# Kernel optimization log

Measured on AMD Instinct MI355X. Metric: run time of the kernel, lower is better.

Reference implementation:

```python
import jax, jax.numpy as jnp
import numpy as np

DIM = 384
NUM_HEADS = 12
HEAD_DIM = DIM // NUM_HEADS
SCALE = HEAD_DIM ** -0.5


def setup_inputs() -> dict:
    key = jax.random.key(0)
    k_x, k_w, k_o = jax.random.split(key, 3)
    B, n, N, C = 2, 64, 256, DIM
    x = jax.random.normal(k_x, (B, n, N, C), dtype=jnp.float32)
    # kaiming_uniform_(a=sqrt(5)) on a (3C, C) matrix -> bound = 1/sqrt(C)
    bound = 1.0 / np.sqrt(C)
    in_proj_weight = jax.random.uniform(k_w, (3 * C, C), dtype=jnp.float32, minval=-bound, maxval=bound)
    in_proj_bias = jnp.zeros((3 * C,), dtype=jnp.float32)
    ob = 1.0 / np.sqrt(C)
    out_proj_weight = jax.random.uniform(k_o, (C, C), dtype=jnp.float32, minval=-ob, maxval=ob)
    return {"x": x, "in_proj_weight": in_proj_weight, "in_proj_bias": in_proj_bias,
            "out_proj_weight": out_proj_weight}


def reference(x, in_proj_weight, in_proj_bias, out_proj_weight):
    B, n, N, C = x.shape
    H, d = NUM_HEADS, C // NUM_HEADS
    # fused QKV projection: F.linear(x, W, b) = x @ W.T + b
    qkv = jnp.einsum('bwnc,oc->bwno', x, in_proj_weight) + in_proj_bias
    q, k, v = jnp.split(qkv, 3, axis=-1)                      # each [B, n, N, C]
    # [B, n, N, C] -> [B, n, H, N, d]
    def heads(t):
        return t.reshape(B, n, N, H, d).transpose(0, 1, 3, 2, 4)
    q = heads(q) * SCALE
    k = heads(k)
    v = heads(v)
    attn = jax.nn.softmax(jnp.einsum('bwhqd,bwhkd->bwhqk', q, k), axis=-1)
    out = jnp.einsum('bwhqk,bwhkd->bwhqd', attn, v)           # [B, n, H, N, d]
    out = out.transpose(0, 1, 3, 2, 4).reshape(B, n, N, C)
    out = jnp.einsum('bwnc,oc->bwno', out, out_proj_weight)   # out_proj has no bias
    return out
```

## Files before the change

### kernel.cpp

```cpp
#include <hip/hip_runtime.h>
#include <hip/hip_bf16.h>

typedef __attribute__((ext_vector_type(4)))  float  f32x4;
typedef __attribute__((ext_vector_type(16))) float  f32x16;
typedef __attribute__((ext_vector_type(8)))  short  bf16x8;
typedef __attribute__((ext_vector_type(8)))  ushort u16x8;

#define C_DIM   384
#define QKV_DIM 1152
#define NHEAD   12
#define HDIM    32
#define NTOK    256

__device__ __forceinline__ ushort f2bf(float f) {
    union { __hip_bfloat16 h; ushort u; } cv;
    cv.h = __float2bfloat16(f);
    return cv.u;
}

__global__ void cvt_kernel(const float* __restrict__ in, ushort* __restrict__ out, int n4) {
    int i = blockIdx.x * blockDim.x + threadIdx.x;
    if (i >= n4) return;
    const float4 v = reinterpret_cast<const float4*>(in)[i];
    ushort4 o;
    o.x = f2bf(v.x); o.y = f2bf(v.y); o.z = f2bf(v.z); o.w = f2bf(v.w);
    reinterpret_cast<ushort4*>(out)[i] = o;
}

template<int BIAS, int OUTF32, int AHB, int OHB>
__global__ __launch_bounds__(256, 3) void gemm_bt(const ushort* __restrict__ A,
                                                  const ushort* __restrict__ Bw,
                                                  const float* __restrict__ bias,
                                                  void* __restrict__ Cout,
                                                  int M, int N, int K) {
    __shared__ __align__(16) ushort As[2][128 * 64];
    __shared__ __align__(16) ushort Bs[2][64 * 64];

    const int t    = threadIdx.x;
    const int lane = t & 63;
    const int wave = t >> 6;
    const int wr   = (wave >> 1) * 64;
    const int wc   = (wave & 1) * 32;
    const int lr   = lane & 15;
    const int lg   = lane >> 4;

    const int gx  = gridDim.x;
    const int nwg = gx * gridDim.y;
    const int hw  = blockIdx.y * gx + blockIdx.x;
    const int cpx = nwg >> 3;
    const int lin = (hw & 7) * cpx + (hw >> 3);
    const int by  = lin / gx;
    const int bx  = lin - by * gx;
    const int mBase = by * 128;
    const int nBase = bx * 64;

    f32x4 acc[4][2] = {};
    const int nK = K >> 6;

    auto stage = [&](int kt, int c) {
        const int k0 = kt << 6;
#pragma unroll
        for (int it = 0; it < 4; ++it) {
            const int idx = it * 256 + t;
            const int r   = idx >> 3;
            const int cb  = (idx & 7) ^ (r & 7);
            const ushort* ga;
            if (AHB) {
                const int k = k0 + cb * 8;
                ga = A + ((size_t)(k >> 5) * M + (mBase + r)) * 32 + (k & 31);
            } else {
                ga = A + (size_t)(mBase + r) * K + k0 + cb * 8;
            }
            __builtin_amdgcn_global_load_lds(
                (const __attribute__((address_space(1))) void*)ga,
                (__attribute__((address_space(3))) void*)(&As[c][it * 2048 + wave * 512]),
                16, 0, 0);
        }
#pragma unroll
        for (int it = 0; it < 2; ++it) {
            const int idx = it * 256 + t;
            const int r   = idx >> 3;
            const int cb  = (idx & 7) ^ (r & 7);
            const ushort* gb = Bw + (size_t)(nBase + r) * K + k0 + cb * 8;
            __builtin_amdgcn_global_load_lds(
                (const __attribute__((address_space(1))) void*)gb,
                (__attribute__((address_space(3))) void*)(&Bs[c][it * 2048 + wave * 512]),
                16, 0, 0);
        }
    };

    stage(0, 0);
    int cur = 0;

    for (int kt = 0; kt < nK; ++kt) {
        if (kt + 1 < nK) {
            stage(kt + 1, cur ^ 1);
            asm volatile("s_waitcnt vmcnt(6)" ::: "memory");
        } else {
            asm volatile("s_waitcnt vmcnt(0)" ::: "memory");
        }
        __builtin_amdgcn_s_barrier();
        __builtin_amdgcn_sched_barrier(0);

#pragma unroll
        for (int kk = 0; kk < 2; ++kk) {
            bf16x8 af[4], bfr[2];
#pragma unroll
            for (int m = 0; m < 4; ++m) {
                const int r = wr + m * 16 + lr;
                af[m] = *reinterpret_cast<const bf16x8*>(
                    &As[cur][r * 64 + (((kk * 4 + lg) ^ (r & 7)) << 3)]);
            }
#pragma unroll
            for (int n = 0; n < 2; ++n) {
                const int r = wc + n * 16 + lr;
                bfr[n] = *reinterpret_cast<const bf16x8*>(
                    &Bs[cur][r * 64 + (((kk * 4 + lg) ^ (r & 7)) << 3)]);
            }
#pragma unroll
            for (int m = 0; m < 4; ++m)
#pragma unroll
                for (int n = 0; n < 2; ++n)
                    acc[m][n] = __builtin_amdgcn_mfma_f32_16x16x32_bf16(af[m], bfr[n], acc[m][n], 0, 0, 0);
        }

        __builtin_amdgcn_sched_barrier(0);
        __builtin_amdgcn_s_barrier();
        cur ^= 1;
    }

#pragma unroll
    for (int n = 0; n < 2; ++n) {
        const int col = nBase + wc + n * 16 + lr;
        const float bv = BIAS ? bias[col] : 0.f;
        const int sel  = OHB ? (col / 384) : 0;
        const int c384 = OHB ? (col - sel * 384) : 0;
#pragma unroll
        for (int m = 0; m < 4; ++m) {
            const int row0 = mBase + wr + m * 16 + lg * 4;
#pragma unroll
            for (int j = 0; j < 4; ++j) {
                const float v = acc[m][n][j] + bv;
                const int row = row0 + j;
                if (OUTF32) {
                    reinterpret_cast<float*>(Cout)[(size_t)row * N + col] = v;
                } else if (OHB) {
                    reinterpret_cast<ushort*>(Cout)[
                        ((size_t)(sel * NHEAD + (c384 >> 5)) * M + row) * 32 + (c384 & 31)] = f2bf(v);
                } else {
                    reinterpret_cast<ushort*>(Cout)[(size_t)row * N + col] = f2bf(v);
                }
            }
        }
    }
}

__global__ __launch_bounds__(512) void attn_kernel(const ushort* __restrict__ qkv,
                                                   ushort* __restrict__ att,
                                                   int Mtok) {
    __shared__ __align__(16) ushort Ks[NTOK * HDIM];
    __shared__ __align__(16) ushort Vt[HDIM * NTOK];

    const int bid = blockIdx.x;
    const int win = bid / NHEAD;
    const int h   = bid % NHEAD;

    const int t    = threadIdx.x;
    const int lane = t & 63;
    const int wave = t >> 6;
    const int l31  = lane & 31;
    const int h5   = lane >> 5;

    const size_t winRow = (size_t)win * NTOK;
    const ushort* Qbase = qkv + ((size_t)h * Mtok + winRow) * HDIM;
    const ushort* Kbase = qkv + ((size_t)(NHEAD + h) * Mtok + winRow) * HDIM;
    const ushort* Vbase = qkv + ((size_t)(2 * NHEAD + h) * Mtok + winRow) * HDIM;

#pragma unroll
    for (int it = 0; it < 2; ++it) {
        const int idx = it * 512 + t;
        const int key = idx >> 2;
        const int cb  = (idx & 3) ^ (key & 3);
        const ushort* gk = Kbase + key * HDIM + cb * 8;
        __builtin_amdgcn_global_load_lds(
            (const __attribute__((address_space(1))) void*)gk,
            (__attribute__((address_space(3))) void*)(&Ks[it * 4096 + wave * 512]),
            16, 0, 0);
    }
#pragma unroll
    for (int it = 0; it < 2; ++it) {
        const int idx = it * 512 + t;
        const int key = idx >> 2;
        const int cb  = idx & 3;
        u16x8 v8 = *reinterpret_cast<const u16x8*>(Vbase + key * HDIM + cb * 8);
#pragma unroll
        for (int jj = 0; jj < 8; ++jj) {
            const int dd  = cb * 8 + jj;
            const int blk = (key >> 3) ^ (dd & 7) ^ ((2 * (dd >> 3)) & 6);
            Vt[dd * NTOK + blk * 8 + (key & 7)] = v8[jj];
        }
    }
    __syncthreads();

    const float c1   = 0.25503509f;
    const int   vmsk = (l31 & 7) ^ ((2 * (l31 >> 3)) & 6);
    const int   kmsk = l31 & 3;
    const int   q0   = wave * 32;

    const int qrow = q0 + l31;
    const bf16x8 qf0 = *reinterpret_cast<const bf16x8*>(
        Qbase + (size_t)qrow * HDIM + h5 * 8);
    const bf16x8 qf1 = *reinterpret_cast<const bf16x8*>(
        Qbase + (size_t)qrow * HDIM + 16 + h5 * 8);

    float sm0 = 0.f, sm1 = 0.f, sm2 = 0.f, sm3 = 0.f;
#pragma unroll
    for (int tt = 0; tt < 8; ++tt) {
        const int key = tt * 32 + l31;
        const bf16x8 kf0 = *reinterpret_cast<const bf16x8*>(
            &Ks[key * HDIM + ((h5 ^ kmsk) << 3)]);
        const bf16x8 kf1 = *reinterpret_cast<const bf16x8*>(
            &Ks[key * HDIM + (((2 + h5) ^ kmsk) << 3)]);
        f32x16 s = {};
        s = __builtin_amdgcn_mfma_f32_32x32x16_bf16(kf0, qf0, s, 0, 0, 0);
        s = __builtin_amdgcn_mfma_f32_32x32x16_bf16(kf1, qf1, s, 0, 0, 0);
#pragma unroll
        for (int r = 0; r < 16; r += 4) {
            sm0 += __builtin_amdgcn_exp2f(s[r + 0] * c1);
            sm1 += __builtin_amdgcn_exp2f(s[r + 1] * c1);
            sm2 += __builtin_amdgcn_exp2f(s[r + 2] * c1);
            sm3 += __builtin_amdgcn_exp2f(s[r + 3] * c1);
        }
    }
    float sm = (sm0 + sm1) + (sm2 + sm3);
    sm += __shfl_xor(sm, 32, 64);
    const float inv = __builtin_amdgcn_rcpf(sm);

    f32x16 O = {};
#pragma unroll
    for (int tt = 0; tt < 8; ++tt) {
        const int key = tt * 32 + l31;
        const bf16x8 kf0 = *reinterpret_cast<const bf16x8*>(
            &Ks[key * HDIM + ((h5 ^ kmsk) << 3)]);
        const bf16x8 kf1 = *reinterpret_cast<const bf16x8*>(
            &Ks[key * HDIM + (((2 + h5) ^ kmsk) << 3)]);
        f32x16 s = {};
        s = __builtin_amdgcn_mfma_f32_32x32x16_bf16(kf0, qf0, s, 0, 0, 0);
        s = __builtin_amdgcn_mfma_f32_32x32x16_bf16(kf1, qf1, s, 0, 0, 0);

        uint pk8[8];
#pragma unroll
        for (int m = 0; m < 8; ++m) {
            const int r = 4 * (m >> 1) + 2 * (m & 1);
            const float lo = __builtin_amdgcn_exp2f(s[r + 0] * c1) * inv;
            const float hi = __builtin_amdgcn_exp2f(s[r + 1] * c1) * inv;
            uint d;
            asm("v_cvt_pk_bf16_f32 %0, %1, %2" : "=v"(d) : "v"(lo), "v"(hi));
            pk8[m] = d;
        }

#pragma unroll
        for (int k16 = 0; k16 < 2; ++k16) {
            const int mb = 4 * k16;
            const uint s0 = h5 ? pk8[mb + 0] : pk8[mb + 2];
            const uint s1 = h5 ? pk8[mb + 1] : pk8[mb + 3];
            const uint x0 = (uint)__shfl_xor((int)s0, 32, 64);
            const uint x1 = (uint)__shfl_xor((int)s1, 32, 64);
            union { uint u[4]; bf16x8 v; } pw;
            pw.u[0] = h5 ? x0 : pk8[mb + 0];
            pw.u[1] = h5 ? x1 : pk8[mb + 1];
            pw.u[2] = h5 ? pk8[mb + 2] : x0;
            pw.u[3] = h5 ? pk8[mb + 3] : x1;
            const int blk = (4 * tt + 2 * k16 + h5) ^ vmsk;
            const bf16x8 vf = *reinterpret_cast<const bf16x8*>(
                &Vt[l31 * NTOK + blk * 8]);
            O = __builtin_amdgcn_mfma_f32_32x32x16_bf16(pw.v, vf, O, 0, 0, 0);
        }
    }

    ushort* obase = att + ((size_t)h * Mtok + winRow + q0) * HDIM + l31;
#pragma unroll
    for (int r = 0; r < 16; ++r) {
        const int qr = (r & 3) + 8 * (r >> 2) + 4 * h5;
        obase[(size_t)qr * HDIM] = f2bf(O[r]);
    }
}

extern "C" void kernel_launch(void* const* d_in, const int* in_sizes, int n_in,
                              void* d_out, int out_size, void* d_ws, size_t ws_size,
                              hipStream_t stream) {
    const float* x     = (const float*)d_in[0];
    const float* w_in  = (const float*)d_in[1];
    const float* b_in  = (const float*)d_in[2];
    const float* w_out = (const float*)d_in[3];

    const int M    = in_sizes[0] / C_DIM;
    const int nWin = M / NTOK;

    char* ws = (char*)d_ws;
    size_t off = 0;
    ushort* xb    = (ushort*)(ws + off); off += (size_t)M * C_DIM * 2;
    ushort* qkvb  = (ushort*)(ws + off); off += (size_t)M * QKV_DIM * 2;
    ushort* attb  = (ushort*)(ws + off); off += (size_t)M * C_DIM * 2;
    ushort* wqkvb = (ushort*)(ws + off); off += (size_t)QKV_DIM * C_DIM * 2;
    ushort* woutb = (ushort*)(ws + off);

    cvt_kernel<<<(M * C_DIM / 4 + 255) / 256, 256, 0, stream>>>(x, xb, M * C_DIM / 4);
    cvt_kernel<<<(QKV_DIM * C_DIM / 4 + 255) / 256, 256, 0, stream>>>(w_in, wqkvb, QKV_DIM * C_DIM / 4);
    cvt_kernel<<<(C_DIM * C_DIM / 4 + 255) / 256, 256, 0, stream>>>(w_out, woutb, C_DIM * C_DIM / 4);

    gemm_bt<1, 0, 0, 1><<<dim3(QKV_DIM / 64, M / 128), 256, 0, stream>>>(
        xb, wqkvb, b_in, qkvb, M, QKV_DIM, C_DIM);

    attn_kernel<<<nWin * NHEAD, 512, 0, stream>>>(qkvb, attb, M);

    gemm_bt<0, 1, 1, 0><<<dim3(C_DIM / 64, M / 128), 256, 0, stream>>>(
        attb, woutb, nullptr, d_out, M, C_DIM, C_DIM);
}
```

Measured before the change: 119.6 us.

## Fuse fp32-to-bf16 input conversion into QKV GEMM A-tile loading

Drops the separate kernel that converted x to bf16. The QKV GEMM now loads fp32 x tiles into registers, converts them to bf16 and writes them into swizzled LDS, with a register-prefetch double buffer overlapping the next tile's loads with the current compute. This removes one full read and write pass over the activation tensor and one launch. In exchange, the A operand no longer uses async global-to-LDS loads, which costs more register pressure and VALU conversion work inside the GEMM. Each column block also reads fp32 A, twice the bytes of bf16.

```diff
diff --git a/kernel.cpp b/kernel.cpp
--- a/kernel.cpp
+++ b/kernel.cpp
@@ -27,14 +27,17 @@
     reinterpret_cast<ushort4*>(out)[i] = o;
 }
 
-template<int BIAS, int OUTF32, int AHB, int OHB>
-__global__ __launch_bounds__(256, 3) void gemm_bt(const ushort* __restrict__ A,
+template<int BIAS, int OUTF32, int AHB, int OHB, int AF32>
+__global__ __launch_bounds__(256, 3) void gemm_bt(const void* __restrict__ Ap,
                                                   const ushort* __restrict__ Bw,
                                                   const float* __restrict__ bias,
                                                   void* __restrict__ Cout,
                                                   int M, int N, int K) {
     __shared__ __align__(16) ushort As[2][128 * 64];
     __shared__ __align__(16) ushort Bs[2][64 * 64];
+
+    const ushort* Ab = (const ushort*)Ap;
+    const float*  Af = (const float*)Ap;
 
     const int t    = threadIdx.x;
     const int lane = t & 63;
@@ -57,25 +60,8 @@
     f32x4 acc[4][2] = {};
     const int nK = K >> 6;
 
-    auto stage = [&](int kt, int c) {
+    auto issueB = [&](int kt, int c) {
         const int k0 = kt << 6;
-#pragma unroll
-        for (int it = 0; it < 4; ++it) {
-            const int idx = it * 256 + t;
-            const int r   = idx >> 3;
-            const int cb  = (idx & 7) ^ (r & 7);
-            const ushort* ga;
-            if (AHB) {
-                const int k = k0 + cb * 8;
-                ga = A + ((size_t)(k >> 5) * M + (mBase + r)) * 32 + (k & 31);
-            } else {
-                ga = A + (size_t)(mBase + r) * K + k0 + cb * 8;
-            }
-            __builtin_amdgcn_global_load_lds(
-                (const __attribute__((address_space(1))) void*)ga,
-                (__attribute__((address_space(3))) void*)(&As[c][it * 2048 + wave * 512]),
-                16, 0, 0);
-        }
 #pragma unroll
         for (int it = 0; it < 2; ++it) {
             const int idx = it * 256 + t;
@@ -89,19 +75,7 @@
         }
     };
 
-    stage(0, 0);
-    int cur = 0;
-
-    for (int kt = 0; kt < nK; ++kt) {
-        if (kt + 1 < nK) {
-            stage(kt + 1, cur ^ 1);
-            asm volatile("s_waitcnt vmcnt(6)" ::: "memory");
-        } else {
-            asm volatile("s_waitcnt vmcnt(0)" ::: "memory");
-        }
-        __builtin_amdgcn_s_barrier();
-        __builtin_amdgcn_sched_barrier(0);
-
+    auto compute = [&](int c) {
 #pragma unroll
         for (int kk = 0; kk < 2; ++kk) {
             bf16x8 af[4], bfr[2];
@@ -109,13 +83,13 @@
             for (int m = 0; m < 4; ++m) {
                 const int r = wr + m * 16 + lr;
                 af[m] = *reinterpret_cast<const bf16x8*>(
-                    &As[cur][r * 64 + (((kk * 4 + lg) ^ (r & 7)) << 3)]);
+                    &As[c][r * 64 + (((kk * 4 + lg) ^ (r & 7)) << 3)]);
             }
 #pragma unroll
             for (int n = 0; n < 2; ++n) {
                 const int r = wc + n * 16 + lr;
                 bfr[n] = *reinterpret_cast<const bf16x8*>(
-                    &Bs[cur][r * 64 + (((kk * 4 + lg) ^ (r & 7)) << 3)]);
+                    &Bs[c][r * 64 + (((kk * 4 + lg) ^ (r & 7)) << 3)]);
             }
 #pragma unroll
             for (int m = 0; m < 4; ++m)
@@ -123,10 +97,86 @@
                 for (int n = 0; n < 2; ++n)
                     acc[m][n] = __builtin_amdgcn_mfma_f32_16x16x32_bf16(af[m], bfr[n], acc[m][n], 0, 0, 0);
         }
-
-        __builtin_amdgcn_sched_barrier(0);
-        __builtin_amdgcn_s_barrier();
-        cur ^= 1;
+    };
+
+    if constexpr (AF32) {
+        float4 a0[4], a1[4];
+        auto ldA = [&](int kt) {
+            const int k0 = kt << 6;
+#pragma unroll
+            for (int it = 0; it < 4; ++it) {
+                const int idx = it * 256 + t;
+                const int r   = idx >> 3;
+                const int cb  = (idx & 7) ^ (r & 7);
+                const float* ga = Af + (size_t)(mBase + r) * K + k0 + cb * 8;
+                a0[it] = *reinterpret_cast<const float4*>(ga);
+                a1[it] = *reinterpret_cast<const float4*>(ga + 4);
+            }
+        };
+        auto wrA = [&](int c) {
+#pragma unroll
+            for (int it = 0; it < 4; ++it) {
+                const int idx = it * 256 + t;
+                union { ushort u[8]; u16x8 v; } pw;
+                pw.u[0] = f2bf(a0[it].x); pw.u[1] = f2bf(a0[it].y);
+                pw.u[2] = f2bf(a0[it].z); pw.u[3] = f2bf(a0[it].w);
+                pw.u[4] = f2bf(a1[it].x); pw.u[5] = f2bf(a1[it].y);
+                pw.u[6] = f2bf(a1[it].z); pw.u[7] = f2bf(a1[it].w);
+                *reinterpret_cast<u16x8*>(&As[c][(size_t)idx * 8]) = pw.v;
+            }
+        };
+
+        ldA(0); issueB(0, 0); wrA(0);
+        __syncthreads();
+        int cur = 0;
+        for (int kt = 0; kt < nK; ++kt) {
+            const bool more = (kt + 1 < nK);
+            if (more) { ldA(kt + 1); issueB(kt + 1, cur ^ 1); }
+            compute(cur);
+            if (more) wrA(cur ^ 1);
+            __syncthreads();
+            cur ^= 1;
+        }
+    } else {
+        auto issueA = [&](int kt, int c) {
+            const int k0 = kt << 6;
+#pragma unroll
+            for (int it = 0; it < 4; ++it) {
+                const int idx = it * 256 + t;
+                const int r   = idx >> 3;
+                const int cb  = (idx & 7) ^ (r & 7);
+                const ushort* ga;
+                if (AHB) {
+                    const int k = k0 + cb * 8;
+                    ga = Ab + ((size_t)(k >> 5) * M + (mBase + r)) * 32 + (k & 31);
+                } else {
+                    ga = Ab + (size_t)(mBase + r) * K + k0 + cb * 8;
+                }
+                __builtin_amdgcn_global_load_lds(
+                    (const __attribute__((address_space(1))) void*)ga,
+                    (__attribute__((address_space(3))) void*)(&As[c][it * 2048 + wave * 512]),
+                    16, 0, 0);
+            }
+        };
+
+        issueA(0, 0); issueB(0, 0);
+        int cur = 0;
+        for (int kt = 0; kt < nK; ++kt) {
+            if (kt + 1 < nK) {
+                issueA(kt + 1, cur ^ 1); issueB(kt + 1, cur ^ 1);
+                asm volatile("s_waitcnt vmcnt(6)" ::: "memory");
+            } else {
+                asm volatile("s_waitcnt vmcnt(0)" ::: "memory");
+            }
+            __builtin_amdgcn_s_barrier();
+            __builtin_amdgcn_sched_barrier(0);
+
+            compute(cur);
+
+            __builtin_amdgcn_sched_barrier(0);
+            __builtin_amdgcn_s_barrier();
+            cur ^= 1;
+        }
     }
 
 #pragma unroll
@@ -299,21 +349,19 @@
 
     char* ws = (char*)d_ws;
     size_t off = 0;
-    ushort* xb    = (ushort*)(ws + off); off += (size_t)M * C_DIM * 2;
     ushort* qkvb  = (ushort*)(ws + off); off += (size_t)M * QKV_DIM * 2;
     ushort* attb  = (ushort*)(ws + off); off += (size_t)M * C_DIM * 2;
     ushort* wqkvb = (ushort*)(ws + off); off += (size_t)QKV_DIM * C_DIM * 2;
     ushort* woutb = (ushort*)(ws + off);
 
-    cvt_kernel<<<(M * C_DIM / 4 + 255) / 256, 256, 0, stream>>>(x, xb, M * C_DIM / 4);
     cvt_kernel<<<(QKV_DIM * C_DIM / 4 + 255) / 256, 256, 0, stream>>>(w_in, wqkvb, QKV_DIM * C_DIM / 4);
     cvt_kernel<<<(C_DIM * C_DIM / 4 + 255) / 256, 256, 0, stream>>>(w_out, woutb, C_DIM * C_DIM / 4);
 
-    gemm_bt<1, 0, 0, 1><<<dim3(QKV_DIM / 64, M / 128), 256, 0, stream>>>(
-        xb, wqkvb, b_in, qkvb, M, QKV_DIM, C_DIM);
+    gemm_bt<1, 0, 0, 1, 1><<<dim3(QKV_DIM / 64, M / 128), 256, 0, stream>>>(
+        x, wqkvb, b_in, qkvb, M, QKV_DIM, C_DIM);
 
     attn_kernel<<<nWin * NHEAD, 512, 0, stream>>>(qkvb, attb, M);
 
-    gemm_bt<0, 1, 1, 0><<<dim3(C_DIM / 64, M / 128), 256, 0, stream>>>(
+    gemm_bt<0, 1, 1, 0, 0><<<dim3(C_DIM / 64, M / 128), 256, 0, stream>>>(
         attb, woutb, nullptr, d_out, M, C_DIM, C_DIM);
 }
```

New measurement: 124.9 us. 4.5% more time.
